# Performance work log

Measured on AMD Instinct MI355X. Metric: run time of the kernel, lower is better.

The kernel has to match this reference:

```python
import jax, jax.numpy as jnp
import numpy as np

T, D, H = 2048, 2048, 2048
HD = H // 2                      # hidden per direction
NTAGS = 20
K = NTAGS + 2                    # + END_TAG, + START_TAG (appended in that order)
END, START = NTAGS, NTAGS + 1
NEG = -10000.0


def setup_inputs() -> dict:
    key = jax.random.key(0)
    ks = jax.random.split(key, 16)
    n = jax.random.normal
    s = 0.02
    trans = n(ks[0], (K, K), dtype=jnp.float32)
    trans = trans.at[START, :].set(NEG).at[:, END].set(NEG)
    return {
        "sequence": n(ks[1], (T, D), dtype=jnp.float32),
        "h0": n(ks[2], (2, HD), dtype=jnp.float32),   # [direction, HD], batch=1 squeezed
        "c0": n(ks[3], (2, HD), dtype=jnp.float32),
        "Wih_f": n(ks[4], (4 * HD, D), dtype=jnp.float32) * s,
        "Whh_f": n(ks[5], (4 * HD, HD), dtype=jnp.float32) * s,
        "bih_f": n(ks[6], (4 * HD,), dtype=jnp.float32) * s,
        "bhh_f": n(ks[7], (4 * HD,), dtype=jnp.float32) * s,
        "Wih_r": n(ks[8], (4 * HD, D), dtype=jnp.float32) * s,
        "Whh_r": n(ks[9], (4 * HD, HD), dtype=jnp.float32) * s,
        "bih_r": n(ks[10], (4 * HD,), dtype=jnp.float32) * s,
        "bhh_r": n(ks[11], (4 * HD,), dtype=jnp.float32) * s,
        "W_tag": n(ks[12], (K, H), dtype=jnp.float32) * s,
        "b_tag": n(ks[13], (K,), dtype=jnp.float32) * s,
        "transitions": trans,
    }


def _lstm_dir(x, h0, c0, Wih, Whh, b):
    """Single-direction LSTM over x:[T,D]; torch gate order i,f,g,o."""
    def step(carry, xt):
        h, c = carry
        g = xt @ Wih.T + h @ Whh.T + b          # [4*HD]
        i, f, gg, o = jnp.split(g, 4)
        i = jax.nn.sigmoid(i)
        f = jax.nn.sigmoid(f)
        gg = jnp.tanh(gg)
        o = jax.nn.sigmoid(o)
        c = f * c + i * gg
        h = o * jnp.tanh(c)
        return (h, c), h
    _, hs = jax.lax.scan(step, (h0, c0), x)
    return hs                                    # [T, HD]


def _viterbi(feats, transitions):
    """Vectorized Viterbi DP; transitions[next, prev]."""
    init = jnp.full((K,), NEG, dtype=feats.dtype).at[START].set(0.0)

    def step(fv, feat):
        nv = transitions + fv[None, :]           # [K next, K prev]
        bp = jnp.argmax(nv, axis=1)              # backpointer per next tag
        return jnp.max(nv, axis=1) + feat, bp

    fv, bps = jax.lax.scan(step, init, feats)    # bps: [T, K]
    terminal = fv + transitions[END]
    score = jnp.max(terminal)
    best = jnp.argmax(terminal)

    def back(tag, bp):
        return bp[tag], tag                      # emit tag at time t, carry tag at t-1

    _, path = jax.lax.scan(back, best, bps, reverse=True)
    return score, path                           # path: [T] int


def reference(sequence, h0, c0, Wih_f, Whh_f, bih_f, bhh_f,
              Wih_r, Whh_r, bih_r, bhh_r, W_tag, b_tag, transitions):
    hs_f = _lstm_dir(sequence, h0[0], c0[0], Wih_f, Whh_f, bih_f + bhh_f)
    hs_r = _lstm_dir(sequence[::-1], h0[1], c0[1], Wih_r, Whh_r, bih_r + bhh_r)[::-1]
    lstm_out = jnp.concatenate([hs_f, hs_r], axis=-1)   # [T, H]
    feats = lstm_out @ W_tag.T + b_tag                  # [T, K]
    score, path = _viterbi(feats, transitions)
    return score, path
```

## Files before the change

### kernel.cpp

```cpp
#include <hip/hip_runtime.h>
#include <hip/hip_bf16.h>
#include <stdint.h>

#define TT 2048
#define DD 2048
#define HDIM 1024
#define G4 4096
#define KTAG 22
#define END_TAG 20
#define START_TAG 21
#define NEGV (-10000.0f)
#define VNEG (-1e30f)
#define VC 64
#define VL 32

typedef __attribute__((ext_vector_type(8))) short bf16x8;
typedef __attribute__((ext_vector_type(4))) float f32x4;

__device__ __forceinline__ float sigm(float x) { return 1.0f / (1.0f + __expf(-x)); }
__device__ __forceinline__ float tanh_fast(float x) {
    float e = __expf(2.0f * x);
    return 1.0f - 2.0f / (e + 1.0f);
}
__device__ __forceinline__ unsigned bf16_bits(float f) {
    unsigned x = __float_as_uint(f);
    return (x + 0x7FFFu + ((x >> 16) & 1u)) >> 16;
}

__global__ void convert_bf16_k(const float* __restrict__ src, __hip_bfloat16* __restrict__ dst, int n) {
    int i = blockIdx.x * blockDim.x + threadIdx.x;
    int stride = gridDim.x * blockDim.x;
    for (; i < n; i += stride) dst[i] = __float2bfloat16(src[i]);
}

__global__ void make_bias_k(const float* __restrict__ bih_f, const float* __restrict__ bhh_f,
                            const float* __restrict__ bih_r, const float* __restrict__ bhh_r,
                            float* __restrict__ ball) {
    int j = blockIdx.x * 256 + threadIdx.x;
    if (j < G4) ball[j] = bih_f[j] + bhh_f[j];
    else if (j < 2 * G4) ball[j] = bih_r[j - G4] + bhh_r[j - G4];
}

#define LDT 40
__global__ __launch_bounds__(256) void gemm_x_k(const __hip_bfloat16* __restrict__ A,
                                                const __hip_bfloat16* __restrict__ B,
                                                const float* __restrict__ bias,
                                                float* __restrict__ X) {
    __shared__ unsigned short As[128 * LDT];
    __shared__ unsigned short Bs[128 * LDT];
    const int tid  = threadIdx.x;
    const int lane = tid & 63;
    const int wave = tid >> 6;
    const int wm = wave >> 1, wn = wave & 1;
    const int m0 = blockIdx.y * 128, n0 = blockIdx.x * 128;
    const int r15 = lane & 15, quad = lane >> 4;

    f32x4 acc[4][4];
#pragma unroll
    for (int i = 0; i < 4; ++i)
#pragma unroll
        for (int j = 0; j < 4; ++j) acc[i][j] = (f32x4){0.f, 0.f, 0.f, 0.f};

    for (int kt = 0; kt < DD; kt += 32) {
#pragma unroll
        for (int it = 0; it < 2; ++it) {
            int idx = it * 256 + tid;
            int row = idx >> 2, ch = idx & 3;
            uint4 va = *(const uint4*)(A + (size_t)(m0 + row) * DD + kt + ch * 8);
            *(uint4*)(&As[row * LDT + ch * 8]) = va;
            uint4 vb = *(const uint4*)(B + (size_t)(n0 + row) * DD + kt + ch * 8);
            *(uint4*)(&Bs[row * LDT + ch * 8]) = vb;
        }
        __syncthreads();
        bf16x8 af[4], bfr[4];
#pragma unroll
        for (int i = 0; i < 4; ++i)
            af[i] = *(const bf16x8*)(&As[(wm * 64 + i * 16 + r15) * LDT + quad * 8]);
#pragma unroll
        for (int j = 0; j < 4; ++j)
            bfr[j] = *(const bf16x8*)(&Bs[(wn * 64 + j * 16 + r15) * LDT + quad * 8]);
#pragma unroll
        for (int i = 0; i < 4; ++i)
#pragma unroll
            for (int j = 0; j < 4; ++j)
                acc[i][j] = __builtin_amdgcn_mfma_f32_16x16x32_bf16(af[i], bfr[j], acc[i][j], 0, 0, 0);
        __syncthreads();
    }
#pragma unroll
    for (int i = 0; i < 4; ++i) {
#pragma unroll
        for (int j = 0; j < 4; ++j) {
            int col = n0 + wn * 64 + j * 16 + r15;
            float b = bias[col];
#pragma unroll
            for (int r = 0; r < 4; ++r) {
                int row = m0 + wm * 64 + i * 16 + quad * 4 + r;
                X[(size_t)row * (2 * G4) + col] = acc[i][j][r] + b;
            }
        }
    }
}

__global__ __launch_bounds__(512, 2) void lstm_recur_k(
    const float* __restrict__ Whh_f, const float* __restrict__ Whh_r,
    const float* __restrict__ h0, const float* __restrict__ c0,
    const float* __restrict__ X,
    unsigned long long* pairs,
    float* __restrict__ hs_out)
{
    const int bid = blockIdx.x;
    const int dir = bid & 1;
    const int slice = bid >> 1;
    const int tid = threadIdx.x;
    const int lane = tid & 63;
    const int wave = tid >> 6;

    __shared__ float h_lds[2][8 * 132];

    const float* Whh = dir ? Whh_r : Whh_f;
    unsigned long long* pd = pairs + (size_t)dir * 1024;

    const int ri = lane >> 3, ch = lane & 7;
    const int u = ri & 1;
    const int unit = slice * 16 + wave * 2 + u;
    const int row = (ri >> 1) * HDIM + unit;

    float w[128];
    {
        const float4* wp = (const float4*)(Whh + (size_t)row * HDIM + ch * 128);
#pragma unroll
        for (int i = 0; i < 32; ++i) {
            float4 v = wp[i];
            w[4 * i + 0] = v.x; w[4 * i + 1] = v.y; w[4 * i + 2] = v.z; w[4 * i + 3] = v.w;
        }
    }

    float c_reg = 0.f;
    if (ch == 0 && ri < 2) c_reg = c0[dir * HDIM + unit];

    if (lane == 0) {
        float2 hv = *(const float2*)(h0 + dir * HDIM + slice * 16 + wave * 2);
        unsigned lo = bf16_bits(hv.x);
        unsigned hi = bf16_bits(hv.y);
        __hip_atomic_store(&pd[slice * 8 + wave],
                           ((unsigned long long)hi << 32) | lo,
                           __ATOMIC_RELAXED, __HIP_MEMORY_SCOPE_AGENT);
    }

    const float* Xrow = X + dir * G4 + row;

    for (int t = 0; t < TT; ++t) {
        const int tx = dir ? (TT - 1 - t) : t;
        float xv = Xrow[(size_t)tx * (2 * G4)];

        unsigned long long* pb = pd + (t & 1) * 512;
        const unsigned tg = (unsigned)t & 0xFFFFu;
        unsigned long long v;
        do {
            v = __hip_atomic_load(&pb[tid], __ATOMIC_RELAXED, __HIP_MEMORY_SCOPE_AGENT);
        } while ((((v >> 16) & 0xFFFFu) != tg) | ((unsigned)(v >> 48) != tg));

        float* hl = h_lds[t & 1];
        float2 hw;
        hw.x = __uint_as_float((unsigned)(v & 0xFFFFu) << 16);
        hw.y = __uint_as_float((unsigned)((v >> 32) & 0xFFFFu) << 16);
        *(float2*)(hl + (tid >> 6) * 132 + ((2 * tid) & 127)) = hw;
        __syncthreads();

        const float4* h4 = (const float4*)(hl + ch * 132);
        float a0 = 0.f, a1 = 0.f;
#pragma unroll
        for (int i = 0; i < 32; i += 2) {
            float4 x = h4[i], y = h4[i + 1];
            a0 = fmaf(w[4 * i + 0], x.x, a0); a0 = fmaf(w[4 * i + 1], x.y, a0);
            a0 = fmaf(w[4 * i + 2], x.z, a0); a0 = fmaf(w[4 * i + 3], x.w, a0);
            a1 = fmaf(w[4 * i + 4], y.x, a1); a1 = fmaf(w[4 * i + 5], y.y, a1);
            a1 = fmaf(w[4 * i + 6], y.z, a1); a1 = fmaf(w[4 * i + 7], y.w, a1);
        }
        float g = a0 + a1;
        g += __shfl_xor(g, 1);
        g += __shfl_xor(g, 2);
        g += __shfl_xor(g, 4);
        g += xv;

        float gI = __shfl(g, (0 + u) * 8 + ch);
        float gF = __shfl(g, (2 + u) * 8 + ch);
        float gG = __shfl(g, (4 + u) * 8 + ch);
        float gO = __shfl(g, (6 + u) * 8 + ch);
        float iv = sigm(gI), fv = sigm(gF), gg = tanh_fast(gG), ov = sigm(gO);
        float c = fv * c_reg + iv * gg;
        c_reg = c;
        float h = ov * tanh_fast(c);
        float h1 = __shfl(h, 8);

        if (lane == 0) {
            *(float2*)(hs_out + (size_t)tx * 2048 + dir * HDIM + slice * 16 + wave * 2) =
                make_float2(h, h1);
            unsigned t1 = (unsigned)(t + 1) & 0xFFFFu;
            unsigned lo = (t1 << 16) | bf16_bits(h);
            unsigned hi = (t1 << 16) | bf16_bits(h1);
            __hip_atomic_store(&pd[((t + 1) & 1) * 512 + slice * 8 + wave],
                               ((unsigned long long)hi << 32) | lo,
                               __ATOMIC_RELAXED, __HIP_MEMORY_SCOPE_AGENT);
        }
    }
}

__global__ __launch_bounds__(256) void feats_k(const float* __restrict__ hs,
                                               const float* __restrict__ Wtag,
                                               const float* __restrict__ btag,
                                               float* __restrict__ feats) {
    const int t = blockIdx.x;
    const int lane = threadIdx.x & 63, wave = threadIdx.x >> 6;
    const float* ht = hs + (size_t)t * 2048;
    for (int j = wave; j < KTAG; j += 4) {
        const float* wr = Wtag + (size_t)j * 2048;
        float acc = 0.f;
#pragma unroll
        for (int i = 0; i < 32; ++i) acc += wr[i * 64 + lane] * ht[i * 64 + lane];
#pragma unroll
        for (int off = 32; off; off >>= 1) acc += __shfl_xor(acc, off);
        if (lane == 0) feats[t * KTAG + j] = acc + btag[j];
    }
}

__global__ __launch_bounds__(512) void vit_compose_k(const float* __restrict__ feats,
                                                     const float* __restrict__ trans,
                                                     float* __restrict__ Cmat) {
    __shared__ float c_lds[KTAG * KTAG];
    __shared__ float ft_s[KTAG];
    const int tid = threadIdx.x;
    const int chunk = blockIdx.x;
    const int j = tid / KTAG, n = tid % KTAG;
    const bool act = (tid < KTAG * KTAG);
    float tr_n[KTAG];
    if (act)
#pragma unroll
        for (int p = 0; p < KTAG; ++p) tr_n[p] = trans[n * KTAG + p];
    float c = (act && n == j) ? 0.f : VNEG;
    for (int s = 0; s < VL; ++s) {
        if (act) c_lds[j * KTAG + n] = c;
        if (tid < KTAG) ft_s[tid] = feats[(chunk * VL + s) * KTAG + tid];
        __syncthreads();
        if (act) {
            float m = VNEG;
#pragma unroll
            for (int p = 0; p < KTAG; ++p)
                m = fmaxf(m, tr_n[p] + c_lds[j * KTAG + p]);
            c = m + ft_s[n];
        }
        __syncthreads();
    }
    if (act) Cmat[chunk * KTAG * KTAG + n * KTAG + j] = c;
}

__global__ __launch_bounds__(64) void vit_scan_k(const float* __restrict__ Cmat,
                                                 const float* __restrict__ trans,
                                                 float* __restrict__ fv_start,
                                                 float* __restrict__ scan_out)
{
    const int n = threadIdx.x;
    const bool act = n < KTAG;
    float fv = (act && n == START_TAG) ? 0.f : NEGV;
    for (int i = 0; i < VC; ++i) {
        if (act) fv_start[i * KTAG + n] = fv;
        float Crow[KTAG];
        if (act)
#pragma unroll
            for (int p = 0; p < KTAG; ++p) Crow[p] = Cmat[i * KTAG * KTAG + n * KTAG + p];
        float m = VNEG;
#pragma unroll
        for (int p = 0; p < KTAG; ++p) {
            float fvp = __shfl(fv, p);
            if (act) m = fmaxf(m, Crow[p] + fvp);
        }
        fv = m;
    }
    float term = act ? (fv + trans[END_TAG * KTAG + n]) : VNEG;
    float best = VNEG; int bt = 0;
#pragma unroll
    for (int p = 0; p < KTAG; ++p) {
        float tv = __shfl(term, p);
        if (tv > best) { best = tv; bt = p; }
    }
    if (n == 0) { scan_out[0] = best; scan_out[1] = (float)bt; }
}

__global__ __launch_bounds__(64) void vit_detail_k(const float* __restrict__ feats,
                                                   const float* __restrict__ trans,
                                                   const float* __restrict__ fv_start,
                                                   unsigned char* __restrict__ bps,
                                                   unsigned char* __restrict__ anc)
{
    const int i = blockIdx.x;
    const int n = threadIdx.x;
    const bool act = n < KTAG;
    float tr_n[KTAG];
    if (act)
#pragma unroll
        for (int p = 0; p < KTAG; ++p) tr_n[p] = trans[n * KTAG + p];
    float fv = act ? fv_start[i * KTAG + n] : VNEG;
    int an = n;
    for (int s = 0; s < VL; ++s) {
        int t = i * VL + s;
        float ft = act ? feats[t * KTAG + n] : 0.f;
        float m = VNEG; int bp = 0;
#pragma unroll
        for (int p = 0; p < KTAG; ++p) {
            float fvp = __shfl(fv, p);
            float vv = tr_n[p] + fvp;
            if (act && vv > m) { m = vv; bp = p; }
        }
        fv = m + ft;
        int anew = __shfl(an, bp);
        if (act) {
            an = anew;
            bps[t * KTAG + n] = (unsigned char)bp;
        }
    }
    if (act) anc[i * KTAG + n] = (unsigned char)an;
}

__global__ __launch_bounds__(256) void vit_backtrack_k(const unsigned char* __restrict__ bps,
                                                       const unsigned char* __restrict__ anc,
                                                       const float* __restrict__ scan_out,
                                                       float* __restrict__ out)
{
    __shared__ unsigned char bps_s[TT * KTAG];
    __shared__ unsigned char anc_s[VC * KTAG];
    __shared__ unsigned char chunk_exit[VC];
    __shared__ short path[TT];
    const int tid = threadIdx.x;
    for (int idx = tid * 16; idx < TT * KTAG; idx += 256 * 16)
        *(int4*)(bps_s + idx) = *(const int4*)(bps + idx);
    for (int idx = tid; idx < VC * KTAG; idx += 256) anc_s[idx] = anc[idx];
    __syncthreads();
    if (tid == 0) {
        int tag = (int)scan_out[1];
        for (int i = VC - 1; i >= 0; --i) {
            chunk_exit[i] = (unsigned char)tag;
            tag = anc_s[i * KTAG + tag];
        }
        out[0] = scan_out[0];
    }
    __syncthreads();
    if (tid < VC) {
        int tag = chunk_exit[tid];
        for (int s = VL - 1; s >= 0; --s) {
            int t = tid * VL + s;
            path[t] = (short)tag;
            tag = bps_s[t * KTAG + tag];
        }
    }
    __syncthreads();
    for (int t = tid; t < TT; t += 256) out[1 + t] = (float)path[t];
}

extern "C" void kernel_launch(void* const* d_in, const int* in_sizes, int n_in,
                              void* d_out, int out_size, void* d_ws, size_t ws_size,
                              hipStream_t stream) {
    const float* seq   = (const float*)d_in[0];
    const float* h0    = (const float*)d_in[1];
    const float* c0    = (const float*)d_in[2];
    const float* Wih_f = (const float*)d_in[3];
    const float* Whh_f = (const float*)d_in[4];
    const float* bih_f = (const float*)d_in[5];
    const float* bhh_f = (const float*)d_in[6];
    const float* Wih_r = (const float*)d_in[7];
    const float* Whh_r = (const float*)d_in[8];
    const float* bih_r = (const float*)d_in[9];
    const float* bhh_r = (const float*)d_in[10];
    const float* Wtag  = (const float*)d_in[11];
    const float* btag  = (const float*)d_in[12];
    const float* trans = (const float*)d_in[13];

    char* ws = (char*)d_ws;
    const size_t MB = 1ull << 20;
    const size_t KB = 1ull << 10;
    __hip_bfloat16* seq_bf = (__hip_bfloat16*)(ws);
    __hip_bfloat16* w_bf   = (__hip_bfloat16*)(ws + 8 * MB);
    float* bias  = (float*)(ws + 40 * MB);
    float* X     = (float*)(ws + 41 * MB);
    float* hs    = (float*)(ws + 105 * MB);
    float* feats = (float*)(ws + 121 * MB);
    unsigned long long* pairs = (unsigned long long*)(ws + 122 * MB);
    float* Cmat     = (float*)(ws + 122 * MB + 128 * KB);
    float* fv_start = (float*)(ws + 122 * MB + 256 * KB);
    float* scan_out = (float*)(ws + 122 * MB + 272 * KB);
    unsigned char* bps = (unsigned char*)(ws + 122 * MB + 288 * KB);
    unsigned char* anc = (unsigned char*)(ws + 122 * MB + 352 * KB);

    convert_bf16_k<<<1024, 256, 0, stream>>>(seq, seq_bf, DD * TT);
    convert_bf16_k<<<1024, 256, 0, stream>>>(Wih_f, w_bf, G4 * DD);
    convert_bf16_k<<<1024, 256, 0, stream>>>(Wih_r, w_bf + (size_t)G4 * DD, G4 * DD);
    make_bias_k<<<32, 256, 0, stream>>>(bih_f, bhh_f, bih_r, bhh_r, bias);
    gemm_x_k<<<dim3(64, 16), 256, 0, stream>>>(seq_bf, w_bf, bias, X);

    {
        const float* a0 = Whh_f; const float* a1 = Whh_r;
        const float* a2 = h0;    const float* a3 = c0;
        const float* a4 = X;     unsigned long long* a5 = pairs;
        float* a6 = hs;
        void* args[] = {&a0, &a1, &a2, &a3, &a4, &a5, &a6};
        hipLaunchCooperativeKernel((const void*)lstm_recur_k, dim3(128), dim3(512), args, 0, stream);
    }

    feats_k<<<TT, 256, 0, stream>>>(hs, Wtag, btag, feats);
    vit_compose_k<<<VC, 512, 0, stream>>>(feats, trans, Cmat);
    vit_scan_k<<<1, 64, 0, stream>>>(Cmat, trans, fv_start, scan_out);
    vit_detail_k<<<VC, 64, 0, stream>>>(feats, trans, fv_start, bps, anc);
    vit_backtrack_k<<<1, 256, 0, stream>>>(bps, anc, scan_out, (float*)d_out);
}
```

Baseline: 4.381 ms.

## Fuse input-projection GEMM into cooperative LSTM kernel with per-chunk readiness counters

The separate input-projection GEMM is folded into the cooperative LSTM launch. 128 extra blocks compute X tiles in time-chunk order, alternating front and back chunks so both directions are fed, and bump a per-chunk atomic counter when a tile is done. The recurrence blocks spin on these counters before reading X for the next 128 timesteps, so the GEMM overlaps the serial recurrence instead of running before it. The h-exchange polling loop also keeps three loads in flight. The cost is that GEMM blocks use only half their threads and compete for CUs and memory bandwidth with the latency-bound recurrence, and launch bounds drop to one block per SM.

Measured after the change: 8.728 ms. 1.99x slower.

```diff
diff --git a/kernel.cpp b/kernel.cpp
--- a/kernel.cpp
+++ b/kernel.cpp
@@ -42,80 +42,96 @@
 }
 
 #define LDT 40
-__global__ __launch_bounds__(256) void gemm_x_k(const __hip_bfloat16* __restrict__ A,
-                                                const __hip_bfloat16* __restrict__ B,
-                                                const float* __restrict__ bias,
-                                                float* __restrict__ X) {
-    __shared__ unsigned short As[128 * LDT];
-    __shared__ unsigned short Bs[128 * LDT];
-    const int tid  = threadIdx.x;
-    const int lane = tid & 63;
-    const int wave = tid >> 6;
-    const int wm = wave >> 1, wn = wave & 1;
-    const int m0 = blockIdx.y * 128, n0 = blockIdx.x * 128;
-    const int r15 = lane & 15, quad = lane >> 4;
-
-    f32x4 acc[4][4];
-#pragma unroll
-    for (int i = 0; i < 4; ++i)
-#pragma unroll
-        for (int j = 0; j < 4; ++j) acc[i][j] = (f32x4){0.f, 0.f, 0.f, 0.f};
-
-    for (int kt = 0; kt < DD; kt += 32) {
-#pragma unroll
-        for (int it = 0; it < 2; ++it) {
-            int idx = it * 256 + tid;
-            int row = idx >> 2, ch = idx & 3;
-            uint4 va = *(const uint4*)(A + (size_t)(m0 + row) * DD + kt + ch * 8);
-            *(uint4*)(&As[row * LDT + ch * 8]) = va;
-            uint4 vb = *(const uint4*)(B + (size_t)(n0 + row) * DD + kt + ch * 8);
-            *(uint4*)(&Bs[row * LDT + ch * 8]) = vb;
-        }
-        __syncthreads();
-        bf16x8 af[4], bfr[4];
-#pragma unroll
-        for (int i = 0; i < 4; ++i)
-            af[i] = *(const bf16x8*)(&As[(wm * 64 + i * 16 + r15) * LDT + quad * 8]);
-#pragma unroll
-        for (int j = 0; j < 4; ++j)
-            bfr[j] = *(const bf16x8*)(&Bs[(wn * 64 + j * 16 + r15) * LDT + quad * 8]);
-#pragma unroll
-        for (int i = 0; i < 4; ++i)
-#pragma unroll
-            for (int j = 0; j < 4; ++j)
-                acc[i][j] = __builtin_amdgcn_mfma_f32_16x16x32_bf16(af[i], bfr[j], acc[i][j], 0, 0, 0);
-        __syncthreads();
-    }
-#pragma unroll
-    for (int i = 0; i < 4; ++i) {
-#pragma unroll
-        for (int j = 0; j < 4; ++j) {
-            int col = n0 + wn * 64 + j * 16 + r15;
-            float b = bias[col];
-#pragma unroll
-            for (int r = 0; r < 4; ++r) {
-                int row = m0 + wm * 64 + i * 16 + quad * 4 + r;
-                X[(size_t)row * (2 * G4) + col] = acc[i][j][r] + b;
-            }
-        }
-    }
-}
-
-__global__ __launch_bounds__(512, 2) void lstm_recur_k(
+__global__ __launch_bounds__(512, 1) void lstm_fused_k(
     const float* __restrict__ Whh_f, const float* __restrict__ Whh_r,
     const float* __restrict__ h0, const float* __restrict__ c0,
-    const float* __restrict__ X,
+    const __hip_bfloat16* __restrict__ seq_bf,
+    const __hip_bfloat16* __restrict__ w_bf,
+    const float* __restrict__ bias,
+    float* X,
     unsigned long long* pairs,
+    int* chunk_cnt,
     float* __restrict__ hs_out)
 {
     const int bid = blockIdx.x;
+    const int tid = threadIdx.x;
+
+    __shared__ unsigned short As[128 * LDT];
+    __shared__ unsigned short Bs[128 * LDT];
+    __shared__ float h_lds[2][8 * 132];
+
+    if (bid >= 128) {
+        const int hid = bid - 128;
+        const int lane = tid & 63;
+        const int wave = tid >> 6;
+        const int wm = wave >> 1, wn = wave & 1;
+        const int r15 = lane & 15, quad = lane >> 4;
+        for (int s = hid; s < 1024; s += 128) {
+            const int po = s >> 6;
+            const int chunk = (po & 1) ? (15 - (po >> 1)) : (po >> 1);
+            const int m0 = chunk * 128;
+            const int n0 = (s & 63) * 128;
+            f32x4 acc[4][4];
+#pragma unroll
+            for (int i = 0; i < 4; ++i)
+#pragma unroll
+                for (int j = 0; j < 4; ++j) acc[i][j] = (f32x4){0.f, 0.f, 0.f, 0.f};
+            for (int kt = 0; kt < DD; kt += 32) {
+                if (tid < 256) {
+#pragma unroll
+                    for (int it = 0; it < 2; ++it) {
+                        int idx = it * 256 + tid;
+                        int row = idx >> 2, ch = idx & 3;
+                        uint4 va = *(const uint4*)(seq_bf + (size_t)(m0 + row) * DD + kt + ch * 8);
+                        *(uint4*)(&As[row * LDT + ch * 8]) = va;
+                        uint4 vb = *(const uint4*)(w_bf + (size_t)(n0 + row) * DD + kt + ch * 8);
+                        *(uint4*)(&Bs[row * LDT + ch * 8]) = vb;
+                    }
+                }
+                __syncthreads();
+                if (tid < 256) {
+                    bf16x8 af[4], bfr[4];
+#pragma unroll
+                    for (int i = 0; i < 4; ++i)
+                        af[i] = *(const bf16x8*)(&As[(wm * 64 + i * 16 + r15) * LDT + quad * 8]);
+#pragma unroll
+                    for (int j = 0; j < 4; ++j)
+                        bfr[j] = *(const bf16x8*)(&Bs[(wn * 64 + j * 16 + r15) * LDT + quad * 8]);
+#pragma unroll
+                    for (int i = 0; i < 4; ++i)
+#pragma unroll
+                        for (int j = 0; j < 4; ++j)
+                            acc[i][j] = __builtin_amdgcn_mfma_f32_16x16x32_bf16(af[i], bfr[j], acc[i][j], 0, 0, 0);
+                }
+                __syncthreads();
+            }
+            if (tid < 256) {
+#pragma unroll
+                for (int i = 0; i < 4; ++i) {
+#pragma unroll
+                    for (int j = 0; j < 4; ++j) {
+                        int col = n0 + wn * 64 + j * 16 + r15;
+                        float b = bias[col];
+#pragma unroll
+                        for (int r = 0; r < 4; ++r) {
+                            int row = m0 + wm * 64 + i * 16 + quad * 4 + r;
+                            X[(size_t)row * (2 * G4) + col] = acc[i][j][r] + b;
+                        }
+                    }
+                }
+            }
+            __syncthreads();
+            if (tid == 0)
+                __hip_atomic_fetch_add(&chunk_cnt[chunk], 1, __ATOMIC_RELEASE,
+                                       __HIP_MEMORY_SCOPE_AGENT);
+        }
+        return;
+    }
+
     const int dir = bid & 1;
     const int slice = bid >> 1;
-    const int tid = threadIdx.x;
     const int lane = tid & 63;
     const int wave = tid >> 6;
-
-    __shared__ float h_lds[2][8 * 132];
 
     const float* Whh = dir ? Whh_r : Whh_f;
     unsigned long long* pd = pairs + (size_t)dir * 1024;
@@ -148,22 +164,39 @@
     }
 
     const float* Xrow = X + dir * G4 + row;
+    int fr = 0;
 
     for (int t = 0; t < TT; ++t) {
         const int tx = dir ? (TT - 1 - t) : t;
+
+        {
+            const int cidx = dir ? (15 - (tx >> 7)) : (tx >> 7);
+            while (cidx >= fr) {
+                const int cc = dir ? (15 - fr) : fr;
+                if (__hip_atomic_load(&chunk_cnt[cc], __ATOMIC_RELAXED,
+                                      __HIP_MEMORY_SCOPE_AGENT) == 64) {
+                    __builtin_amdgcn_fence(__ATOMIC_ACQUIRE, "agent");
+                    ++fr;
+                }
+            }
+        }
         float xv = Xrow[(size_t)tx * (2 * G4)];
 
         unsigned long long* pb = pd + (t & 1) * 512;
         const unsigned tg = (unsigned)t & 0xFFFFu;
-        unsigned long long v;
-        do {
-            v = __hip_atomic_load(&pb[tid], __ATOMIC_RELAXED, __HIP_MEMORY_SCOPE_AGENT);
-        } while ((((v >> 16) & 0xFFFFu) != tg) | ((unsigned)(v >> 48) != tg));
+        unsigned long long v0, v1, v2;
+        v0 = __hip_atomic_load(&pb[tid], __ATOMIC_RELAXED, __HIP_MEMORY_SCOPE_AGENT);
+        v1 = __hip_atomic_load(&pb[tid], __ATOMIC_RELAXED, __HIP_MEMORY_SCOPE_AGENT);
+        v2 = __hip_atomic_load(&pb[tid], __ATOMIC_RELAXED, __HIP_MEMORY_SCOPE_AGENT);
+        while ((((v0 >> 16) & 0xFFFFu) != tg) | ((unsigned)(v0 >> 48) != tg)) {
+            v0 = v1; v1 = v2;
+            v2 = __hip_atomic_load(&pb[tid], __ATOMIC_RELAXED, __HIP_MEMORY_SCOPE_AGENT);
+        }
 
         float* hl = h_lds[t & 1];
         float2 hw;
-        hw.x = __uint_as_float((unsigned)(v & 0xFFFFu) << 16);
-        hw.y = __uint_as_float((unsigned)((v >> 32) & 0xFFFFu) << 16);
+        hw.x = __uint_as_float((unsigned)(v0 & 0xFFFFu) << 16);
+        hw.y = __uint_as_float((unsigned)((v0 >> 32) & 0xFFFFu) << 16);
         *(float2*)(hl + (tid >> 6) * 132 + ((2 * tid) & 127)) = hw;
         __syncthreads();
 
@@ -384,25 +417,29 @@
     float* hs    = (float*)(ws + 105 * MB);
     float* feats = (float*)(ws + 121 * MB);
     unsigned long long* pairs = (unsigned long long*)(ws + 122 * MB);
+    int*   chunk_cnt = (int*)(ws + 122 * MB + 64 * KB);
     float* Cmat     = (float*)(ws + 122 * MB + 128 * KB);
     float* fv_start = (float*)(ws + 122 * MB + 256 * KB);
     float* scan_out = (float*)(ws + 122 * MB + 272 * KB);
     unsigned char* bps = (unsigned char*)(ws + 122 * MB + 288 * KB);
     unsigned char* anc = (unsigned char*)(ws + 122 * MB + 352 * KB);
 
+    hipMemsetAsync(chunk_cnt, 0, 16 * sizeof(int), stream);
     convert_bf16_k<<<1024, 256, 0, stream>>>(seq, seq_bf, DD * TT);
     convert_bf16_k<<<1024, 256, 0, stream>>>(Wih_f, w_bf, G4 * DD);
     convert_bf16_k<<<1024, 256, 0, stream>>>(Wih_r, w_bf + (size_t)G4 * DD, G4 * DD);
     make_bias_k<<<32, 256, 0, stream>>>(bih_f, bhh_f, bih_r, bhh_r, bias);
-    gemm_x_k<<<dim3(64, 16), 256, 0, stream>>>(seq_bf, w_bf, bias, X);
 
     {
         const float* a0 = Whh_f; const float* a1 = Whh_r;
         const float* a2 = h0;    const float* a3 = c0;
-        const float* a4 = X;     unsigned long long* a5 = pairs;
-        float* a6 = hs;
-        void* args[] = {&a0, &a1, &a2, &a3, &a4, &a5, &a6};
-        hipLaunchCooperativeKernel((const void*)lstm_recur_k, dim3(128), dim3(512), args, 0, stream);
+        const __hip_bfloat16* a4 = seq_bf;
+        const __hip_bfloat16* a5 = w_bf;
+        const float* a6 = bias;  float* a7 = X;
+        unsigned long long* a8 = pairs;
+        int* a9 = chunk_cnt;     float* a10 = hs;
+        void* args[] = {&a0, &a1, &a2, &a3, &a4, &a5, &a6, &a7, &a8, &a9, &a10};
+        hipLaunchCooperativeKernel((const void*)lstm_fused_k, dim3(256), dim3(512), args, 0, stream);
     }
 
     feats_k<<<TT, 256, 0, stream>>>(hs, Wtag, btag, feats);
```
